# Performance work log

Measured on AMD Instinct MI355X. Metric: run time of the kernel, lower is better.

## Reference

```python
import jax, jax.numpy as jnp
import numpy as np
import math

B, S, D, H, FF, V, L = 8, 1024, 512, 8, 2048, 32000, 6
HD = D // H
EPS = 1e-6


def _positional_encoding(seq_len, d_model):
    pos = np.arange(seq_len, dtype=np.float32)[:, None]
    div = np.exp(np.arange(0, d_model, 2, dtype=np.float32) * (-math.log(10000.0) / d_model))
    pe = np.zeros((seq_len, d_model), dtype=np.float32)
    pe[:, 0::2] = np.sin(pos * div)
    pe[:, 1::2] = np.cos(pos * div)
    return jnp.asarray(pe)[None]  # [1, S, D]


def setup_inputs() -> dict:
    key = jax.random.key(0)
    ks = jax.random.split(key, 10)
    s = 0.02
    return {
        'tokens': jax.random.randint(ks[0], (B, S), 0, V, dtype=jnp.int32),
        'mask': jnp.ones((B, 1, 1, S), dtype=jnp.int32),
        'emb': jax.random.normal(ks[1], (V, D), jnp.float32) * s,
        'Wq': jax.random.normal(ks[2], (D, D), jnp.float32) * s,
        'bq': jnp.zeros((D,), jnp.float32),
        'Wk': jax.random.normal(ks[3], (D, D), jnp.float32) * s,
        'bk': jnp.zeros((D,), jnp.float32),
        'Wv': jax.random.normal(ks[4], (D, D), jnp.float32) * s,
        'bv': jnp.zeros((D,), jnp.float32),
        'Wo': jax.random.normal(ks[5], (D, D), jnp.float32) * s,
        'bo': jnp.zeros((D,), jnp.float32),
        'W1': jax.random.normal(ks[6], (D, FF), jnp.float32) * s,
        'b1': jnp.zeros((FF,), jnp.float32),
        'W2': jax.random.normal(ks[7], (FF, D), jnp.float32) * s,
        'b2': jnp.zeros((D,), jnp.float32),
        'ln_a1': jnp.ones((1,), jnp.float32),
        'ln_b1': jnp.zeros((1,), jnp.float32),
        'ln_a2': jnp.ones((1,), jnp.float32),
        'ln_b2': jnp.zeros((1,), jnp.float32),
    }


def _layernorm(x, alpha, bias):
    # custom LN from source: unbiased std (torch default), scalar alpha/bias,
    # eps added to std (not variance)
    mean = jnp.mean(x, axis=-1, keepdims=True)
    std = jnp.std(x, axis=-1, keepdims=True, ddof=1)
    return alpha * (x - mean) / (std + EPS) + bias


def reference(tokens, mask, emb, Wq, bq, Wk, bk, Wv, bv, Wo, bo,
              W1, b1, W2, b2, ln_a1, ln_b1, ln_a2, ln_b2):
    b, s = tokens.shape
    x = emb[tokens] * jnp.asarray(math.sqrt(D), emb.dtype)  # [B,S,D]
    x = x + _positional_encoding(s, D)
    neg = jnp.asarray(-1e9, x.dtype)
    scale = jnp.asarray(1.0 / math.sqrt(HD), x.dtype)
    # NOTE: source reuses the same EncoderBlock instance -> shared weights per layer
    for _ in range(L):
        # --- self-attention sublayer (pre-norm residual) ---
        h = _layernorm(x, ln_a1, ln_b1)
        q = (h @ Wq + bq).reshape(b, s, H, HD).transpose(0, 2, 1, 3)
        k = (h @ Wk + bk).reshape(b, s, H, HD).transpose(0, 2, 1, 3)
        v = (h @ Wv + bv).reshape(b, s, H, HD).transpose(0, 2, 1, 3)
        scores = jnp.einsum('bhqd,bhkd->bhqk', q, k) * scale
        scores = jnp.where(mask == 0, neg, scores)
        attn = jax.nn.softmax(scores, axis=-1)
        o = jnp.einsum('bhqk,bhkd->bhqd', attn, v)
        o = o.transpose(0, 2, 1, 3).reshape(b, s, D)
        x = x + (o @ Wo + bo)
        # --- feed-forward sublayer (pre-norm residual) ---
        h2 = _layernorm(x, ln_a2, ln_b2)
        x = x + (jax.nn.relu(h2 @ W1 + b1) @ W2 + b2)
    return x
```

## Files before the change

### kernel.cpp

```cpp
#include <hip/hip_runtime.h>
#include <hip/hip_bf16.h>
#include <math.h>

#define BB 8
#define SS 1024
#define DD 512
#define HH 8
#define FF 2048
#define LL 6
#define HD 64
#define MM (BB * SS)
#define EPS 1e-6f

typedef __attribute__((ext_vector_type(8))) short bf16x8;
typedef __attribute__((ext_vector_type(4))) float f32x4;

typedef __attribute__((address_space(1))) const unsigned int g_u32;
typedef __attribute__((address_space(3))) unsigned int l_u32;

__device__ __forceinline__ short f2bf(float f) {
    union { float f; unsigned u; } c; c.f = f;
    unsigned u = c.u;
    u += 0x7fff + ((u >> 16) & 1);
    return (short)(u >> 16);
}

__device__ __forceinline__ void gload_lds16(const void* g, void* l) {
    __builtin_amdgcn_global_load_lds((g_u32*)g, (l_u32*)l, 16, 0, 0);
}

__global__ __launch_bounds__(256) void embed_pe_kernel(
    const int* __restrict__ tokens, const float* __restrict__ emb,
    float* __restrict__ x)
{
    int idx = blockIdx.x * 256 + threadIdx.x;
    int d  = idx & (DD - 1);
    int bs = idx >> 9;
    int s  = bs & (SS - 1);
    int tok = tokens[bs];
    float val = emb[(size_t)tok * DD + d] * 22.62741699796952f;
    int i2 = d & ~1;
    float freq = expf((float)i2 * -0.017988946039015984f);
    float ang = (float)s * freq;
    val += (d & 1) ? cosf(ang) : sinf(ang);
    x[idx] = val;
}

__global__ __launch_bounds__(256) void wcvt_kernel(
    const float* __restrict__ W, short* __restrict__ Wt, int K, int N)
{
    __shared__ float tile[32][33];
    int n0 = blockIdx.x * 32, k0 = blockIdx.y * 32;
    int tx = threadIdx.x & 31, ty = threadIdx.x >> 5;
    #pragma unroll
    for (int i = 0; i < 4; ++i)
        tile[ty + i * 8][tx] = W[(size_t)(k0 + ty + i * 8) * N + n0 + tx];
    __syncthreads();
    #pragma unroll
    for (int i = 0; i < 4; ++i)
        Wt[(size_t)(n0 + ty + i * 8) * K + k0 + tx] = f2bf(tile[tx][ty + i * 8]);
}

__global__ __launch_bounds__(256) void ln_kernel(
    const float* __restrict__ x, short* __restrict__ y,
    const float* __restrict__ alpha_p, const float* __restrict__ beta_p)
{
    int row = blockIdx.x;
    const float* xr = x + (size_t)row * DD;
    int t = threadIdx.x;
    float v0 = xr[t];
    float v1 = xr[t + 256];

    __shared__ float red[8];
    float s = v0 + v1;
    #pragma unroll
    for (int o = 32; o >= 1; o >>= 1) s += __shfl_xor(s, o, 64);
    int wid = t >> 6;
    if ((t & 63) == 0) red[wid] = s;
    __syncthreads();
    float mean = (red[0] + red[1] + red[2] + red[3]) * (1.0f / 512.0f);

    float d0 = v0 - mean, d1 = v1 - mean;
    float q = d0 * d0 + d1 * d1;
    #pragma unroll
    for (int o = 32; o >= 1; o >>= 1) q += __shfl_xor(q, o, 64);
    if ((t & 63) == 0) red[4 + wid] = q;
    __syncthreads();
    float var = (red[4] + red[5] + red[6] + red[7]) * (1.0f / 511.0f);
    float stdv = sqrtf(var);

    float alpha = alpha_p[0], beta = beta_p[0];
    float inv = alpha / (stdv + EPS);
    short* yr = y + (size_t)row * DD;
    yr[t]       = f2bf(d0 * inv + beta);
    yr[t + 256] = f2bf(d1 * inv + beta);
}

template <bool RELU, bool RES, bool OUT_BF16>
__global__ __launch_bounds__(256) void gemm_mfma(
    const short* __restrict__ A, const short* __restrict__ Wt,
    const float* __restrict__ bias, const float* __restrict__ R,
    void* __restrict__ Cout, int M, int N, int K)
{
    __shared__ __align__(16) short As[128 * 64];
    __shared__ __align__(16) short Bs[128 * 64];

    const int t = threadIdx.x;
    const int w = t >> 6, l = t & 63;
    const int l15 = l & 15, l4 = l >> 4;
    const int wr = w >> 1, wc = w & 1;

    const int m0 = blockIdx.y * 128, n0 = blockIdx.x * 128;

    f32x4 acc[4][4];
    #pragma unroll
    for (int mi = 0; mi < 4; ++mi)
        #pragma unroll
        for (int ni = 0; ni < 4; ++ni) acc[mi][ni] = (f32x4){0.f, 0.f, 0.f, 0.f};

    const int lrow = l >> 3;
    const int lcol = (l & 7) * 8;

    for (int k0 = 0; k0 < K; k0 += 64) {
        #pragma unroll
        for (int i = 0; i < 4; ++i) {
            int r0 = (w * 4 + i) * 8;
            gload_lds16(A  + (size_t)(m0 + r0 + lrow) * K + k0 + lcol, &As[r0 * 64]);
            gload_lds16(Wt + (size_t)(n0 + r0 + lrow) * K + k0 + lcol, &Bs[r0 * 64]);
        }
        __syncthreads();

        #pragma unroll
        for (int ks = 0; ks < 2; ++ks) {
            bf16x8 af[4], bf_[4];
            #pragma unroll
            for (int mi = 0; mi < 4; ++mi)
                af[mi] = *(const bf16x8*)&As[(wr * 64 + mi * 16 + l15) * 64 + ks * 32 + l4 * 8];
            #pragma unroll
            for (int ni = 0; ni < 4; ++ni)
                bf_[ni] = *(const bf16x8*)&Bs[(wc * 64 + ni * 16 + l15) * 64 + ks * 32 + l4 * 8];
            #pragma unroll
            for (int mi = 0; mi < 4; ++mi)
                #pragma unroll
                for (int ni = 0; ni < 4; ++ni)
                    acc[mi][ni] = __builtin_amdgcn_mfma_f32_16x16x32_bf16(
                        af[mi], bf_[ni], acc[mi][ni], 0, 0, 0);
        }
        __syncthreads();
    }

    #pragma unroll
    for (int mi = 0; mi < 4; ++mi) {
        #pragma unroll
        for (int ni = 0; ni < 4; ++ni) {
            int col = n0 + wc * 64 + ni * 16 + l15;
            float bcol = bias[col];
            #pragma unroll
            for (int r = 0; r < 4; ++r) {
                int row = m0 + wr * 64 + mi * 16 + l4 * 4 + r;
                float c = acc[mi][ni][r] + bcol;
                if (RES)  c += R[(size_t)row * N + col];
                if (RELU) c = fmaxf(c, 0.0f);
                if (OUT_BF16) ((short*)Cout)[(size_t)row * N + col] = f2bf(c);
                else          ((float*)Cout)[(size_t)row * N + col] = c;
            }
        }
    }
}

#define SWZ(row, col) (((row) * 64 + (col)) ^ (((row) & 7) << 3))

__global__ __launch_bounds__(256) void attn_mfma_kernel(
    const short* __restrict__ q, const short* __restrict__ k,
    const short* __restrict__ v, const int* __restrict__ mask,
    short* __restrict__ o)
{
    __shared__ __align__(16) short Ks[64 * 64];
    __shared__ __align__(16) short Vt[64 * 64];
    __shared__ __align__(16) short Ps[4][32 * 64];

    const int qt = blockIdx.x;
    const int bh = blockIdx.y;
    const int b = bh >> 3, h = bh & 7;

    const int t = threadIdx.x;
    const int w = t >> 6;
    const int l = t & 63;
    const int l15 = l & 15, l4 = l >> 4;

    const short* kb = k + ((size_t)b * SS) * DD + h * HD;
    const short* vb = v + ((size_t)b * SS) * DD + h * HD;
    const int*   mb = mask + (size_t)b * SS;
    const int qbase = qt * 128 + w * 32;

    bf16x8 qf[2][2];
    #pragma unroll
    for (int qs = 0; qs < 2; ++qs)
        #pragma unroll
        for (int ks = 0; ks < 2; ++ks)
            qf[qs][ks] = *(const bf16x8*)(q + ((size_t)b * SS + qbase + qs * 16 + l15) * DD
                                          + h * HD + ks * 32 + l4 * 8);

    float m_run[2][4], l_run[2][4];
    f32x4 O[2][4];
    #pragma unroll
    for (int qs = 0; qs < 2; ++qs)
        #pragma unroll
        for (int r = 0; r < 4; ++r) { m_run[qs][r] = -1e30f; l_run[qs][r] = 0.0f; }
    #pragma unroll
    for (int qs = 0; qs < 2; ++qs)
        #pragma unroll
        for (int ds = 0; ds < 4; ++ds) O[qs][ds] = (f32x4){0.f, 0.f, 0.f, 0.f};

    short* Pw = Ps[w];
    const int srow = t >> 2;
    const int scol = (t & 3) * 16;

    for (int kt = 0; kt < SS / 64; ++kt) {
        {
            const short* kp = kb + (size_t)(kt * 64 + srow) * DD + scol;
            bf16x8 k0v = *(const bf16x8*)kp;
            bf16x8 k1v = *(const bf16x8*)(kp + 8);
            *(bf16x8*)&Ks[SWZ(srow, scol)]     = k0v;
            *(bf16x8*)&Ks[SWZ(srow, scol + 8)] = k1v;

            const short* vp = vb + (size_t)(kt * 64 + srow) * DD + scol;
            bf16x8 v0v = *(const bf16x8*)vp;
            bf16x8 v1v = *(const bf16x8*)(vp + 8);
            #pragma unroll
            for (int j = 0; j < 8; ++j) {
                Vt[SWZ(scol + j,     srow)] = v0v[j];
                Vt[SWZ(scol + 8 + j, srow)] = v1v[j];
            }
        }
        __syncthreads();

        f32x4 S[2][4];
        #pragma unroll
        for (int qs = 0; qs < 2; ++qs)
            #pragma unroll
            for (int ku = 0; ku < 4; ++ku) S[qs][ku] = (f32x4){0.f, 0.f, 0.f, 0.f};
        #pragma unroll
        for (int ks = 0; ks < 2; ++ks) {
            bf16x8 kf[4];
            #pragma unroll
            for (int ku = 0; ku < 4; ++ku)
                kf[ku] = *(const bf16x8*)&Ks[SWZ(l15 + 16 * ku, ks * 32 + l4 * 8)];
            #pragma unroll
            for (int qs = 0; qs < 2; ++qs)
                #pragma unroll
                for (int ku = 0; ku < 4; ++ku)
                    S[qs][ku] = __builtin_amdgcn_mfma_f32_16x16x32_bf16(
                        qf[qs][ks], kf[ku], S[qs][ku], 0, 0, 0);
        }

        int mv[4];
        #pragma unroll
        for (int ku = 0; ku < 4; ++ku) mv[ku] = mb[kt * 64 + ku * 16 + l15];

        float p[2][4][4];
        #pragma unroll
        for (int qs = 0; qs < 2; ++qs)
            #pragma unroll
            for (int ku = 0; ku < 4; ++ku)
                #pragma unroll
                for (int r = 0; r < 4; ++r) {
                    float sv = S[qs][ku][r] * 0.125f;
                    p[qs][ku][r] = (mv[ku] == 0) ? -1e9f : sv;
                }

        #pragma unroll
        for (int qs = 0; qs < 2; ++qs)
            #pragma unroll
            for (int r = 0; r < 4; ++r) {
                float mx = fmaxf(fmaxf(p[qs][0][r], p[qs][1][r]),
                                 fmaxf(p[qs][2][r], p[qs][3][r]));
                mx = fmaxf(mx, __shfl_xor(mx, 1, 64));
                mx = fmaxf(mx, __shfl_xor(mx, 2, 64));
                mx = fmaxf(mx, __shfl_xor(mx, 4, 64));
                mx = fmaxf(mx, __shfl_xor(mx, 8, 64));
                float mnew = fmaxf(m_run[qs][r], mx);
                float sc_old = __expf(m_run[qs][r] - mnew);
                m_run[qs][r] = mnew;
                float ps = 0.0f;
                #pragma unroll
                for (int ku = 0; ku < 4; ++ku) {
                    float e = __expf(p[qs][ku][r] - mnew);
                    p[qs][ku][r] = e;
                    ps += e;
                }
                ps += __shfl_xor(ps, 1, 64);
                ps += __shfl_xor(ps, 2, 64);
                ps += __shfl_xor(ps, 4, 64);
                ps += __shfl_xor(ps, 8, 64);
                l_run[qs][r] = l_run[qs][r] * sc_old + ps;
                #pragma unroll
                for (int ds = 0; ds < 4; ++ds) O[qs][ds][r] *= sc_old;
            }

        #pragma unroll
        for (int qs = 0; qs < 2; ++qs)
            #pragma unroll
            for (int ku = 0; ku < 4; ++ku)
                #pragma unroll
                for (int r = 0; r < 4; ++r)
                    Pw[SWZ(qs * 16 + l4 * 4 + r, ku * 16 + l15)] = f2bf(p[qs][ku][r]);

        #pragma unroll
        for (int ks = 0; ks < 2; ++ks) {
            bf16x8 vf[4];
            #pragma unroll
            for (int ds = 0; ds < 4; ++ds)
                vf[ds] = *(const bf16x8*)&Vt[SWZ(l15 + 16 * ds, ks * 32 + l4 * 8)];
            #pragma unroll
            for (int qs = 0; qs < 2; ++qs) {
                bf16x8 pf = *(const bf16x8*)&Pw[SWZ(qs * 16 + l15, ks * 32 + l4 * 8)];
                #pragma unroll
                for (int ds = 0; ds < 4; ++ds)
                    O[qs][ds] = __builtin_amdgcn_mfma_f32_16x16x32_bf16(
                        pf, vf[ds], O[qs][ds], 0, 0, 0);
            }
        }
        __syncthreads();
    }

    #pragma unroll
    for (int qs = 0; qs < 2; ++qs)
        #pragma unroll
        for (int r = 0; r < 4; ++r) {
            float inv = 1.0f / l_run[qs][r];
            int qrow = qbase + qs * 16 + l4 * 4 + r;
            short* orow = o + ((size_t)b * SS + qrow) * DD + h * HD;
            #pragma unroll
            for (int ds = 0; ds < 4; ++ds)
                orow[ds * 16 + l15] = f2bf(O[qs][ds][r] * inv);
        }
}

extern "C" void kernel_launch(void* const* d_in, const int* in_sizes, int n_in,
                              void* d_out, int out_size, void* d_ws, size_t ws_size,
                              hipStream_t stream)
{
    const int*   tokens = (const int*)  d_in[0];
    const int*   mask   = (const int*)  d_in[1];
    const float* emb    = (const float*)d_in[2];
    const float* Wq     = (const float*)d_in[3];
    const float* bq     = (const float*)d_in[4];
    const float* Wk     = (const float*)d_in[5];
    const float* bk     = (const float*)d_in[6];
    const float* Wv     = (const float*)d_in[7];
    const float* bv     = (const float*)d_in[8];
    const float* Wo     = (const float*)d_in[9];
    const float* bo     = (const float*)d_in[10];
    const float* W1     = (const float*)d_in[11];
    const float* b1     = (const float*)d_in[12];
    const float* W2     = (const float*)d_in[13];
    const float* b2     = (const float*)d_in[14];
    const float* ln_a1  = (const float*)d_in[15];
    const float* ln_b1  = (const float*)d_in[16];
    const float* ln_a2  = (const float*)d_in[17];
    const float* ln_b2  = (const float*)d_in[18];

    float* x = (float*)d_out;

    char* p = (char*)d_ws;
    const size_t ACT2 = (size_t)MM * DD * 2;
    short* h   = (short*)p;                 p += ACT2;
    short* qb  = (short*)p;                 p += ACT2;
    short* kb  = (short*)p;                 p += ACT2;
    short* vb  = (short*)p;                 p += ACT2;
    short* ff  = (short*)p;                 p += (size_t)MM * FF * 2;
    short* Wqt = (short*)p;                 p += (size_t)DD * DD * 2;
    short* Wkt = (short*)p;                 p += (size_t)DD * DD * 2;
    short* Wvt = (short*)p;                 p += (size_t)DD * DD * 2;
    short* Wot = (short*)p;                 p += (size_t)DD * DD * 2;
    short* W1t = (short*)p;                 p += (size_t)DD * FF * 2;
    short* W2t = (short*)p;                 p += (size_t)FF * DD * 2;

    embed_pe_kernel<<<(MM * DD) / 256, 256, 0, stream>>>(tokens, emb, x);

    wcvt_kernel<<<dim3(DD / 32, DD / 32), 256, 0, stream>>>(Wq, Wqt, DD, DD);
    wcvt_kernel<<<dim3(DD / 32, DD / 32), 256, 0, stream>>>(Wk, Wkt, DD, DD);
    wcvt_kernel<<<dim3(DD / 32, DD / 32), 256, 0, stream>>>(Wv, Wvt, DD, DD);
    wcvt_kernel<<<dim3(DD / 32, DD / 32), 256, 0, stream>>>(Wo, Wot, DD, DD);
    wcvt_kernel<<<dim3(FF / 32, DD / 32), 256, 0, stream>>>(W1, W1t, DD, FF);
    wcvt_kernel<<<dim3(DD / 32, FF / 32), 256, 0, stream>>>(W2, W2t, FF, DD);

    dim3 gD(DD / 128, MM / 128);
    dim3 gF(FF / 128, MM / 128);
    dim3 gA(SS / 128, BB * HH);

    for (int layer = 0; layer < LL; ++layer) {
        ln_kernel<<<MM, 256, 0, stream>>>(x, h, ln_a1, ln_b1);
        gemm_mfma<false, false, true><<<gD, 256, 0, stream>>>(h, Wqt, bq, nullptr, qb, MM, DD, DD);
        gemm_mfma<false, false, true><<<gD, 256, 0, stream>>>(h, Wkt, bk, nullptr, kb, MM, DD, DD);
        gemm_mfma<false, false, true><<<gD, 256, 0, stream>>>(h, Wvt, bv, nullptr, vb, MM, DD, DD);
        attn_mfma_kernel<<<gA, 256, 0, stream>>>(qb, kb, vb, mask, h);
        gemm_mfma<false, true, false><<<gD, 256, 0, stream>>>(h, Wot, bo, x, x, MM, DD, DD);

        ln_kernel<<<MM, 256, 0, stream>>>(x, h, ln_a2, ln_b2);
        gemm_mfma<true, false, true><<<gF, 256, 0, stream>>>(h, W1t, b1, nullptr, ff, MM, FF, DD);
        gemm_mfma<false, true, false><<<gD, 256, 0, stream>>>(ff, W2t, b2, x, x, MM, DD, FF);
    }
}
```

Measured before the change: 1.489 ms.

## Fuse QKV projections, narrow N-tiles for D-output GEMMs, retile attention and LN

Concatenates Wq/Wk/Wv (and biases) into a single 1536-wide weight so one GEMM writes an interleaved qkv buffer, and attention reads Q/K/V from it with stride 1536. The D-output GEMMs (Wo, W2) use 128x64 tiles to double block count and fill more CUs. Attention moves to 512 threads, with each wave owning 16 query rows instead of 32, which lowers registers per wave. LayerNorm handles two rows per block with float4 loads. The aim is fewer launches and better occupancy, at the cost of less reuse per wave in attention.

After: 1.407 ms. 1.06x faster.

```diff
diff --git a/kernel.cpp b/kernel.cpp
--- a/kernel.cpp
+++ b/kernel.cpp
@@ -11,6 +11,7 @@
 #define HD 64
 #define MM (BB * SS)
 #define EPS 1e-6f
+#define QKVS 1536
 
 typedef __attribute__((ext_vector_type(8))) short bf16x8;
 typedef __attribute__((ext_vector_type(4))) float f32x4;
@@ -61,62 +62,76 @@
         Wt[(size_t)(n0 + ty + i * 8) * K + k0 + tx] = f2bf(tile[tx][ty + i * 8]);
 }
 
+__global__ __launch_bounds__(256) void bcat_kernel(
+    const float* __restrict__ bq, const float* __restrict__ bk,
+    const float* __restrict__ bv, float* __restrict__ out)
+{
+    int i = blockIdx.x * 256 + threadIdx.x;
+    float v = (i < 512) ? bq[i] : (i < 1024 ? bk[i - 512] : bv[i - 1024]);
+    out[i] = v;
+}
+
 __global__ __launch_bounds__(256) void ln_kernel(
     const float* __restrict__ x, short* __restrict__ y,
     const float* __restrict__ alpha_p, const float* __restrict__ beta_p)
 {
-    int row = blockIdx.x;
+    int t = threadIdx.x;
+    int half = t >> 7, i = t & 127;
+    int row = blockIdx.x * 2 + half;
     const float* xr = x + (size_t)row * DD;
-    int t = threadIdx.x;
-    float v0 = xr[t];
-    float v1 = xr[t + 256];
+    float4 v = *(const float4*)(xr + i * 4);
 
     __shared__ float red[8];
-    float s = v0 + v1;
+    float s = v.x + v.y + v.z + v.w;
     #pragma unroll
     for (int o = 32; o >= 1; o >>= 1) s += __shfl_xor(s, o, 64);
-    int wid = t >> 6;
-    if ((t & 63) == 0) red[wid] = s;
+    int wv = t >> 6;
+    if ((t & 63) == 0) red[wv] = s;
     __syncthreads();
-    float mean = (red[0] + red[1] + red[2] + red[3]) * (1.0f / 512.0f);
-
-    float d0 = v0 - mean, d1 = v1 - mean;
-    float q = d0 * d0 + d1 * d1;
+    float mean = (red[half * 2] + red[half * 2 + 1]) * (1.0f / 512.0f);
+
+    float d0 = v.x - mean, d1 = v.y - mean, d2 = v.z - mean, d3 = v.w - mean;
+    float q = d0 * d0 + d1 * d1 + d2 * d2 + d3 * d3;
     #pragma unroll
     for (int o = 32; o >= 1; o >>= 1) q += __shfl_xor(q, o, 64);
-    if ((t & 63) == 0) red[4 + wid] = q;
+    if ((t & 63) == 0) red[4 + wv] = q;
     __syncthreads();
-    float var = (red[4] + red[5] + red[6] + red[7]) * (1.0f / 511.0f);
+    float var = (red[4 + half * 2] + red[5 + half * 2]) * (1.0f / 511.0f);
     float stdv = sqrtf(var);
 
     float alpha = alpha_p[0], beta = beta_p[0];
     float inv = alpha / (stdv + EPS);
-    short* yr = y + (size_t)row * DD;
-    yr[t]       = f2bf(d0 * inv + beta);
-    yr[t + 256] = f2bf(d1 * inv + beta);
-}
-
-template <bool RELU, bool RES, bool OUT_BF16>
+    short4 ov;
+    ov.x = f2bf(d0 * inv + beta); ov.y = f2bf(d1 * inv + beta);
+    ov.z = f2bf(d2 * inv + beta); ov.w = f2bf(d3 * inv + beta);
+    *(short4*)(y + (size_t)row * DD + i * 4) = ov;
+}
+
+template <int BN, bool RELU, bool RES, bool OUT_BF16>
 __global__ __launch_bounds__(256) void gemm_mfma(
     const short* __restrict__ A, const short* __restrict__ Wt,
     const float* __restrict__ bias, const float* __restrict__ R,
     void* __restrict__ Cout, int M, int N, int K)
 {
     __shared__ __align__(16) short As[128 * 64];
-    __shared__ __align__(16) short Bs[128 * 64];
+    __shared__ __align__(16) short Bs[BN * 64];
+
+    constexpr int MI = (BN == 128) ? 4 : 2;
+    constexpr int NI = 4;
 
     const int t = threadIdx.x;
     const int w = t >> 6, l = t & 63;
     const int l15 = l & 15, l4 = l >> 4;
-    const int wr = w >> 1, wc = w & 1;
-
-    const int m0 = blockIdx.y * 128, n0 = blockIdx.x * 128;
-
-    f32x4 acc[4][4];
-    #pragma unroll
-    for (int mi = 0; mi < 4; ++mi)
-        #pragma unroll
-        for (int ni = 0; ni < 4; ++ni) acc[mi][ni] = (f32x4){0.f, 0.f, 0.f, 0.f};
+    const int wrow = (BN == 128) ? (w >> 1) * 64 : w * 32;
+    const int wcol = (BN == 128) ? (w & 1) * 64 : 0;
+
+    const int m0 = blockIdx.y * 128, n0 = blockIdx.x * BN;
+
+    f32x4 acc[MI][NI];
+    #pragma unroll
+    for (int mi = 0; mi < MI; ++mi)
+        #pragma unroll
+        for (int ni = 0; ni < NI; ++ni) acc[mi][ni] = (f32x4){0.f, 0.f, 0.f, 0.f};
 
     const int lrow = l >> 3;
     const int lcol = (l & 7) * 8;
@@ -125,24 +140,28 @@
         #pragma unroll
         for (int i = 0; i < 4; ++i) {
             int r0 = (w * 4 + i) * 8;
-            gload_lds16(A  + (size_t)(m0 + r0 + lrow) * K + k0 + lcol, &As[r0 * 64]);
+            gload_lds16(A + (size_t)(m0 + r0 + lrow) * K + k0 + lcol, &As[r0 * 64]);
+        }
+        #pragma unroll
+        for (int i = 0; i < BN / 32; ++i) {
+            int r0 = (w * (BN / 32) + i) * 8;
             gload_lds16(Wt + (size_t)(n0 + r0 + lrow) * K + k0 + lcol, &Bs[r0 * 64]);
         }
         __syncthreads();
 
         #pragma unroll
         for (int ks = 0; ks < 2; ++ks) {
-            bf16x8 af[4], bf_[4];
-            #pragma unroll
-            for (int mi = 0; mi < 4; ++mi)
-                af[mi] = *(const bf16x8*)&As[(wr * 64 + mi * 16 + l15) * 64 + ks * 32 + l4 * 8];
-            #pragma unroll
-            for (int ni = 0; ni < 4; ++ni)
-                bf_[ni] = *(const bf16x8*)&Bs[(wc * 64 + ni * 16 + l15) * 64 + ks * 32 + l4 * 8];
-            #pragma unroll
-            for (int mi = 0; mi < 4; ++mi)
+            bf16x8 af[MI], bf_[NI];
+            #pragma unroll
+            for (int mi = 0; mi < MI; ++mi)
+                af[mi] = *(const bf16x8*)&As[(wrow + mi * 16 + l15) * 64 + ks * 32 + l4 * 8];
+            #pragma unroll
+            for (int ni = 0; ni < NI; ++ni)
+                bf_[ni] = *(const bf16x8*)&Bs[(wcol + ni * 16 + l15) * 64 + ks * 32 + l4 * 8];
+            #pragma unroll
+            for (int mi = 0; mi < MI; ++mi)
                 #pragma unroll
-                for (int ni = 0; ni < 4; ++ni)
+                for (int ni = 0; ni < NI; ++ni)
                     acc[mi][ni] = __builtin_amdgcn_mfma_f32_16x16x32_bf16(
                         af[mi], bf_[ni], acc[mi][ni], 0, 0, 0);
         }
@@ -150,14 +169,14 @@
     }
 
     #pragma unroll
-    for (int mi = 0; mi < 4; ++mi) {
-        #pragma unroll
-        for (int ni = 0; ni < 4; ++ni) {
-            int col = n0 + wc * 64 + ni * 16 + l15;
+    for (int mi = 0; mi < MI; ++mi) {
+        #pragma unroll
+        for (int ni = 0; ni < NI; ++ni) {
+            int col = n0 + wcol + ni * 16 + l15;
             float bcol = bias[col];
             #pragma unroll
             for (int r = 0; r < 4; ++r) {
-                int row = m0 + wr * 64 + mi * 16 + l4 * 4 + r;
+                int row = m0 + wrow + mi * 16 + l4 * 4 + r;
                 float c = acc[mi][ni][r] + bcol;
                 if (RES)  c += R[(size_t)row * N + col];
                 if (RELU) c = fmaxf(c, 0.0f);
@@ -170,14 +189,13 @@
 
 #define SWZ(row, col) (((row) * 64 + (col)) ^ (((row) & 7) << 3))
 
-__global__ __launch_bounds__(256) void attn_mfma_kernel(
-    const short* __restrict__ q, const short* __restrict__ k,
-    const short* __restrict__ v, const int* __restrict__ mask,
+__global__ __launch_bounds__(512, 4) void attn_mfma_kernel(
+    const short* __restrict__ qkv, const int* __restrict__ mask,
     short* __restrict__ o)
 {
     __shared__ __align__(16) short Ks[64 * 64];
     __shared__ __align__(16) short Vt[64 * 64];
-    __shared__ __align__(16) short Ps[4][32 * 64];
+    __shared__ __align__(16) short Ps[8][16 * 64];
 
     const int qt = blockIdx.x;
     const int bh = blockIdx.y;
@@ -188,58 +206,42 @@
     const int l = t & 63;
     const int l15 = l & 15, l4 = l >> 4;
 
-    const short* kb = k + ((size_t)b * SS) * DD + h * HD;
-    const short* vb = v + ((size_t)b * SS) * DD + h * HD;
+    const short* kb = qkv + ((size_t)b * SS) * QKVS + 512 + h * HD;
+    const short* vb = qkv + ((size_t)b * SS) * QKVS + 1024 + h * HD;
     const int*   mb = mask + (size_t)b * SS;
-    const int qbase = qt * 128 + w * 32;
-
-    bf16x8 qf[2][2];
-    #pragma unroll
-    for (int qs = 0; qs < 2; ++qs)
-        #pragma unroll
-        for (int ks = 0; ks < 2; ++ks)
-            qf[qs][ks] = *(const bf16x8*)(q + ((size_t)b * SS + qbase + qs * 16 + l15) * DD
-                                          + h * HD + ks * 32 + l4 * 8);
-
-    float m_run[2][4], l_run[2][4];
-    f32x4 O[2][4];
-    #pragma unroll
-    for (int qs = 0; qs < 2; ++qs)
-        #pragma unroll
-        for (int r = 0; r < 4; ++r) { m_run[qs][r] = -1e30f; l_run[qs][r] = 0.0f; }
-    #pragma unroll
-    for (int qs = 0; qs < 2; ++qs)
-        #pragma unroll
-        for (int ds = 0; ds < 4; ++ds) O[qs][ds] = (f32x4){0.f, 0.f, 0.f, 0.f};
+    const int qbase = qt * 128 + w * 16;
+
+    bf16x8 qf[2];
+    #pragma unroll
+    for (int ks = 0; ks < 2; ++ks)
+        qf[ks] = *(const bf16x8*)(qkv + ((size_t)b * SS + qbase + l15) * QKVS
+                                  + h * HD + ks * 32 + l4 * 8);
+
+    float m_run[4], l_run[4];
+    f32x4 O[4];
+    #pragma unroll
+    for (int r = 0; r < 4; ++r) { m_run[r] = -1e30f; l_run[r] = 0.0f; }
+    #pragma unroll
+    for (int ds = 0; ds < 4; ++ds) O[ds] = (f32x4){0.f, 0.f, 0.f, 0.f};
 
     short* Pw = Ps[w];
-    const int srow = t >> 2;
-    const int scol = (t & 3) * 16;
+    const int srow = t >> 3;
+    const int scol = (t & 7) * 8;
 
     for (int kt = 0; kt < SS / 64; ++kt) {
         {
-            const short* kp = kb + (size_t)(kt * 64 + srow) * DD + scol;
-            bf16x8 k0v = *(const bf16x8*)kp;
-            bf16x8 k1v = *(const bf16x8*)(kp + 8);
-            *(bf16x8*)&Ks[SWZ(srow, scol)]     = k0v;
-            *(bf16x8*)&Ks[SWZ(srow, scol + 8)] = k1v;
-
-            const short* vp = vb + (size_t)(kt * 64 + srow) * DD + scol;
-            bf16x8 v0v = *(const bf16x8*)vp;
-            bf16x8 v1v = *(const bf16x8*)(vp + 8);
-            #pragma unroll
-            for (int j = 0; j < 8; ++j) {
-                Vt[SWZ(scol + j,     srow)] = v0v[j];
-                Vt[SWZ(scol + 8 + j, srow)] = v1v[j];
-            }
+            bf16x8 kv = *(const bf16x8*)(kb + (size_t)(kt * 64 + srow) * QKVS + scol);
+            *(bf16x8*)&Ks[SWZ(srow, scol)] = kv;
+            bf16x8 vv = *(const bf16x8*)(vb + (size_t)(kt * 64 + srow) * QKVS + scol);
+            #pragma unroll
+            for (int j = 0; j < 8; ++j)
+                Vt[SWZ(scol + j, srow)] = vv[j];
         }
         __syncthreads();
 
-        f32x4 S[2][4];
-        #pragma unroll
-        for (int qs = 0; qs < 2; ++qs)
-            #pragma unroll
-            for (int ku = 0; ku < 4; ++ku) S[qs][ku] = (f32x4){0.f, 0.f, 0.f, 0.f};
+        f32x4 S[4];
+        #pragma unroll
+        for (int ku = 0; ku < 4; ++ku) S[ku] = (f32x4){0.f, 0.f, 0.f, 0.f};
         #pragma unroll
         for (int ks = 0; ks < 2; ++ks) {
             bf16x8 kf[4];
@@ -247,64 +249,55 @@
             for (int ku = 0; ku < 4; ++ku)
                 kf[ku] = *(const bf16x8*)&Ks[SWZ(l15 + 16 * ku, ks * 32 + l4 * 8)];
             #pragma unroll
-            for (int qs = 0; qs < 2; ++qs)
-                #pragma unroll
-                for (int ku = 0; ku < 4; ++ku)
-                    S[qs][ku] = __builtin_amdgcn_mfma_f32_16x16x32_bf16(
-                        qf[qs][ks], kf[ku], S[qs][ku], 0, 0, 0);
+            for (int ku = 0; ku < 4; ++ku)
+                S[ku] = __builtin_amdgcn_mfma_f32_16x16x32_bf16(
+                    qf[ks], kf[ku], S[ku], 0, 0, 0);
         }
 
         int mv[4];
         #pragma unroll
         for (int ku = 0; ku < 4; ++ku) mv[ku] = mb[kt * 64 + ku * 16 + l15];
 
-        float p[2][4][4];
-        #pragma unroll
-        for (int qs = 0; qs < 2; ++qs)
-            #pragma unroll
-            for (int ku = 0; ku < 4; ++ku)
-                #pragma unroll
-                for (int r = 0; r < 4; ++r) {
-                    float sv = S[qs][ku][r] * 0.125f;
-                    p[qs][ku][r] = (mv[ku] == 0) ? -1e9f : sv;
-                }
-
-        #pragma unroll
-        for (int qs = 0; qs < 2; ++qs)
+        float p[4][4];
+        #pragma unroll
+        for (int ku = 0; ku < 4; ++ku)
             #pragma unroll
             for (int r = 0; r < 4; ++r) {
-                float mx = fmaxf(fmaxf(p[qs][0][r], p[qs][1][r]),
-                                 fmaxf(p[qs][2][r], p[qs][3][r]));
-                mx = fmaxf(mx, __shfl_xor(mx, 1, 64));
-                mx = fmaxf(mx, __shfl_xor(mx, 2, 64));
-                mx = fmaxf(mx, __shfl_xor(mx, 4, 64));
-                mx = fmaxf(mx, __shfl_xor(mx, 8, 64));
-                float mnew = fmaxf(m_run[qs][r], mx);
-                float sc_old = __expf(m_run[qs][r] - mnew);
-                m_run[qs][r] = mnew;
-                float ps = 0.0f;
-                #pragma unroll
-                for (int ku = 0; ku < 4; ++ku) {
-                    float e = __expf(p[qs][ku][r] - mnew);
-                    p[qs][ku][r] = e;
-                    ps += e;
-                }
-                ps += __shfl_xor(ps, 1, 64);
-                ps += __shfl_xor(ps, 2, 64);
-                ps += __shfl_xor(ps, 4, 64);
-                ps += __shfl_xor(ps, 8, 64);
-                l_run[qs][r] = l_run[qs][r] * sc_old + ps;
-                #pragma unroll
-                for (int ds = 0; ds < 4; ++ds) O[qs][ds][r] *= sc_old;
+                float sv = S[ku][r] * 0.125f;
+                p[ku][r] = (mv[ku] == 0) ? -1e9f : sv;
             }
 
         #pragma unroll
-        for (int qs = 0; qs < 2; ++qs)
-            #pragma unroll
-            for (int ku = 0; ku < 4; ++ku)
-                #pragma unroll
-                for (int r = 0; r < 4; ++r)
-                    Pw[SWZ(qs * 16 + l4 * 4 + r, ku * 16 + l15)] = f2bf(p[qs][ku][r]);
+        for (int r = 0; r < 4; ++r) {
+            float mx = fmaxf(fmaxf(p[0][r], p[1][r]), fmaxf(p[2][r], p[3][r]));
+            mx = fmaxf(mx, __shfl_xor(mx, 1, 64));
+            mx = fmaxf(mx, __shfl_xor(mx, 2, 64));
+            mx = fmaxf(mx, __shfl_xor(mx, 4, 64));
+            mx = fmaxf(mx, __shfl_xor(mx, 8, 64));
+            float mnew = fmaxf(m_run[r], mx);
+            float sc_old = __expf(m_run[r] - mnew);
+            m_run[r] = mnew;
+            float ps = 0.0f;
+            #pragma unroll
+            for (int ku = 0; ku < 4; ++ku) {
+                float e = __expf(p[ku][r] - mnew);
+                p[ku][r] = e;
+                ps += e;
+            }
+            ps += __shfl_xor(ps, 1, 64);
+            ps += __shfl_xor(ps, 2, 64);
+            ps += __shfl_xor(ps, 4, 64);
+            ps += __shfl_xor(ps, 8, 64);
+            l_run[r] = l_run[r] * sc_old + ps;
+            #pragma unroll
+            for (int ds = 0; ds < 4; ++ds) O[ds][r] *= sc_old;
+        }
+
+        #pragma unroll
+        for (int ku = 0; ku < 4; ++ku)
+            #pragma unroll
+            for (int r = 0; r < 4; ++r)
+                Pw[SWZ(l4 * 4 + r, ku * 16 + l15)] = f2bf(p[ku][r]);
 
         #pragma unroll
         for (int ks = 0; ks < 2; ++ks) {
@@ -312,29 +305,24 @@
             #pragma unroll
             for (int ds = 0; ds < 4; ++ds)
                 vf[ds] = *(const bf16x8*)&Vt[SWZ(l15 + 16 * ds, ks * 32 + l4 * 8)];
-            #pragma unroll
-            for (int qs = 0; qs < 2; ++qs) {
-                bf16x8 pf = *(const bf16x8*)&Pw[SWZ(qs * 16 + l15, ks * 32 + l4 * 8)];
-                #pragma unroll
-                for (int ds = 0; ds < 4; ++ds)
-                    O[qs][ds] = __builtin_amdgcn_mfma_f32_16x16x32_bf16(
-                        pf, vf[ds], O[qs][ds], 0, 0, 0);
-            }
+            bf16x8 pf = *(const bf16x8*)&Pw[SWZ(l15, ks * 32 + l4 * 8)];
+            #pragma unroll
+            for (int ds = 0; ds < 4; ++ds)
+                O[ds] = __builtin_amdgcn_mfma_f32_16x16x32_bf16(
+                    pf, vf[ds], O[ds], 0, 0, 0);
         }
         __syncthreads();
     }
 
     #pragma unroll
-    for (int qs = 0; qs < 2; ++qs)
-        #pragma unroll
-        for (int r = 0; r < 4; ++r) {
-            float inv = 1.0f / l_run[qs][r];
-            int qrow = qbase + qs * 16 + l4 * 4 + r;
-            short* orow = o + ((size_t)b * SS + qrow) * DD + h * HD;
-            #pragma unroll
-            for (int ds = 0; ds < 4; ++ds)
-                orow[ds * 16 + l15] = f2bf(O[qs][ds][r] * inv);
-        }
+    for (int r = 0; r < 4; ++r) {
+        float inv = 1.0f / l_run[r];
+        int qrow = qbase + l4 * 4 + r;
+        short* orow = o + ((size_t)b * SS + qrow) * DD + h * HD;
+        #pragma unroll
+        for (int ds = 0; ds < 4; ++ds)
+            orow[ds * 16 + l15] = f2bf(O[ds][r] * inv);
+    }
 }
 
 extern "C" void kernel_launch(void* const* d_in, const int* in_sizes, int n_in,
@@ -364,42 +352,43 @@
     float* x = (float*)d_out;
 
     char* p = (char*)d_ws;
-    const size_t ACT2 = (size_t)MM * DD * 2;
-    short* h   = (short*)p;                 p += ACT2;
-    short* qb  = (short*)p;                 p += ACT2;
-    short* kb  = (short*)p;                 p += ACT2;
-    short* vb  = (short*)p;                 p += ACT2;
-    short* ff  = (short*)p;                 p += (size_t)MM * FF * 2;
-    short* Wqt = (short*)p;                 p += (size_t)DD * DD * 2;
-    short* Wkt = (short*)p;                 p += (size_t)DD * DD * 2;
-    short* Wvt = (short*)p;                 p += (size_t)DD * DD * 2;
-    short* Wot = (short*)p;                 p += (size_t)DD * DD * 2;
-    short* W1t = (short*)p;                 p += (size_t)DD * FF * 2;
-    short* W2t = (short*)p;                 p += (size_t)FF * DD * 2;
+    short* qkv  = (short*)p;  p += (size_t)MM * QKVS * 2;
+    short* h    = (short*)p;  p += (size_t)MM * DD * 2;
+    short* ff   = (short*)p;  p += (size_t)MM * FF * 2;
+    short* Wqkvt= (short*)p;  p += (size_t)QKVS * DD * 2;
+    short* Wot  = (short*)p;  p += (size_t)DD * DD * 2;
+    short* W1t  = (short*)p;  p += (size_t)FF * DD * 2;
+    short* W2t  = (short*)p;  p += (size_t)DD * FF * 2;
+    float* bqkv = (float*)p;  p += QKVS * 4;
 
     embed_pe_kernel<<<(MM * DD) / 256, 256, 0, stream>>>(tokens, emb, x);
 
-    wcvt_kernel<<<dim3(DD / 32, DD / 32), 256, 0, stream>>>(Wq, Wqt, DD, DD);
-    wcvt_kernel<<<dim3(DD / 32, DD / 32), 256, 0, stream>>>(Wk, Wkt, DD, DD);
-    wcvt_kernel<<<dim3(DD / 32, DD / 32), 256, 0, stream>>>(Wv, Wvt, DD, DD);
+    wcvt_kernel<<<dim3(DD / 32, DD / 32), 256, 0, stream>>>(Wq, Wqkvt,            DD, DD);
+    wcvt_kernel<<<dim3(DD / 32, DD / 32), 256, 0, stream>>>(Wk, Wqkvt + 512*512,  DD, DD);
+    wcvt_kernel<<<dim3(DD / 32, DD / 32), 256, 0, stream>>>(Wv, Wqkvt + 1024*512, DD, DD);
     wcvt_kernel<<<dim3(DD / 32, DD / 32), 256, 0, stream>>>(Wo, Wot, DD, DD);
     wcvt_kernel<<<dim3(FF / 32, DD / 32), 256, 0, stream>>>(W1, W1t, DD, FF);
     wcvt_kernel<<<dim3(DD / 32, FF / 32), 256, 0, stream>>>(W2, W2t, FF, DD);
-
-    dim3 gD(DD / 128, MM / 128);
-    dim3 gF(FF / 128, MM / 128);
-    dim3 gA(SS / 128, BB * HH);
+    bcat_kernel<<<QKVS / 256, 256, 0, stream>>>(bq, bk, bv, bqkv);
+
+    dim3 gQKV(QKVS / 128, MM / 128);
+    dim3 gO  (DD / 64,    MM / 128);
+    dim3 gF1 (FF / 128,   MM / 128);
+    dim3 gF2 (DD / 64,    MM / 128);
+    dim3 gA  (SS / 128,   BB * HH);
 
     for (int layer = 0; layer < LL; ++layer) {
-        ln_kernel<<<MM, 256, 0, stream>>>(x, h, ln_a1, ln_b1);
-        gemm_mfma<false, false, true><<<gD, 256, 0, stream>>>(h, Wqt, bq, nullptr, qb, MM, DD, DD);
-        gemm_mfma<false, false, true><<<gD, 256, 0, stream>>>(h, Wkt, bk, nullptr, kb, MM, DD, DD);
-        gemm_mfma<false, false, true><<<gD, 256, 0, stream>>>(h, Wvt, bv, nullptr, vb, MM, DD, DD);
-        attn_mfma_kernel<<<gA, 256, 0, stream>>>(qb, kb, vb, mask, h);
-        gemm_mfma<false, true, false><<<gD, 256, 0, stream>>>(h, Wot, bo, x, x, MM, DD, DD);
-
-        ln_kernel<<<MM, 256, 0, stream>>>(x, h, ln_a2, ln_b2);
-        gemm_mfma<true, false, true><<<gF, 256, 0, stream>>>(h, W1t, b1, nullptr, ff, MM, FF, DD);
-        gemm_mfma<false, true, false><<<gD, 256, 0, stream>>>(ff, W2t, b2, x, x, MM, DD, FF);
-    }
-}
+        ln_kernel<<<MM / 2, 256, 0, stream>>>(x, h, ln_a1, ln_b1);
+        gemm_mfma<128, false, false, true><<<gQKV, 256, 0, stream>>>(
+            h, Wqkvt, bqkv, nullptr, qkv, MM, QKVS, DD);
+        attn_mfma_kernel<<<gA, 512, 0, stream>>>(qkv, mask, h);
+        gemm_mfma<64, false, true, false><<<gO, 256, 0, stream>>>(
+            h, Wot, bo, x, x, MM, DD, DD);
+
+        ln_kernel<<<MM / 2, 256, 0, stream>>>(x, h, ln_a2, ln_b2);
+        gemm_mfma<128, true, false, true><<<gF1, 256, 0, stream>>>(
+            h, W1t, b1, nullptr, ff, MM, FF, DD);
+        gemm_mfma<64, false, true, false><<<gF2, 256, 0, stream>>>(
+            ff, W2t, b2, x, x, MM, DD, FF);
+    }
+}
```
